# Kernel tuning notes

Hardware: AMD Instinct MI355X
Metric: run time of the kernel (lower is better)

The kernel has to match this reference:

```python
import jax, jax.numpy as jnp
import numpy as np

NUM_HEADS = 16
NUM_KV_HEADS = 4
HEAD_DIM = 128
HALF_DIM = HEAD_DIM // 2
LAMBDA_INIT = 0.8
LAMBDA_MIN = 0.0
LAMBDA_MAX = 1.0
CAUSAL = True
NORMALIZE_DIFF = True
NEG = -1.0e9


def setup_inputs() -> dict:
    key = jax.random.key(0)
    k1, k2, k3 = jax.random.split(key, 3)
    B, Sq, Sk = 1, 2048, 2048
    query = jax.random.normal(k1, (B, NUM_HEADS, Sq, HEAD_DIM), dtype=jnp.float32)
    key_t = jax.random.normal(k2, (B, NUM_KV_HEADS, Sk, HEAD_DIM), dtype=jnp.float32)
    value = jax.random.normal(k3, (B, NUM_KV_HEADS, Sk, HEAD_DIM), dtype=jnp.float32)
    return {"query": query, "key": key_t, "value": value}


def reference(query, key, value):
    scale = 1.0 / (HALF_DIM ** 0.5)
    lam = jnp.clip(jnp.float32(LAMBDA_INIT), LAMBDA_MIN, LAMBDA_MAX)
    # GQA: repeat KV heads to match query heads
    rep = NUM_HEADS // NUM_KV_HEADS
    k = jnp.repeat(key, rep, axis=1)    # [b,h,k,d]
    v = jnp.repeat(value, rep, axis=1)  # [b,h,k,d]
    q1, q2 = query[..., :HALF_DIM], query[..., HALF_DIM:]
    k1, k2 = k[..., :HALF_DIM], k[..., HALF_DIM:]
    scores1 = jnp.einsum('bhqd,bhkd->bhqk', q1, k1) * scale
    scores2 = jnp.einsum('bhqd,bhkd->bhqk', q2, k2) * scale
    if CAUSAL:
        Sq, Sk = query.shape[2], k.shape[2]
        mask = jnp.tril(jnp.ones((Sq, Sk), dtype=jnp.float32))  # lower-triangular causal
        scores1 = scores1 * mask + (1.0 - mask) * NEG
        scores2 = scores2 * mask + (1.0 - mask) * NEG
    attn1 = jax.nn.softmax(scores1, axis=-1)
    attn2 = jax.nn.softmax(scores2, axis=-1)
    diff_attn = attn1 - lam * attn2
    out = jnp.einsum('bhqk,bhkd->bhqd', diff_attn, v)
    if NORMALIZE_DIFF:
        out = out * (1.0 - LAMBDA_INIT)
    return out
```

## Files before the change

### kernel.cpp

```cpp
#include <hip/hip_runtime.h>

#define NUM_HEADS 16
#define HEAD_DIM  128
#define SEQ       2048
#define KT_STRIDE 8192

typedef __attribute__((ext_vector_type(8))) unsigned short us8;
typedef __attribute__((ext_vector_type(8))) __bf16 bf16x8;
typedef __attribute__((ext_vector_type(4))) float f32x4;
typedef __attribute__((ext_vector_type(16))) float f32x16;
typedef __attribute__((ext_vector_type(4))) unsigned u32x4;
typedef __attribute__((ext_vector_type(2))) unsigned u32x2;

static __device__ inline unsigned short f2bf(float x) {
    union { float f; unsigned u; } v; v.f = x;
    unsigned r = v.u + 0x7FFFu + ((v.u >> 16) & 1u);
    return (unsigned short)(r >> 16);
}
static __device__ inline unsigned pk2bf(float a, float b) {
    return (unsigned)f2bf(a) | ((unsigned)f2bf(b) << 16);
}
static __device__ inline float fast_exp2(float x) {
#if __has_builtin(__builtin_amdgcn_exp2f)
    return __builtin_amdgcn_exp2f(x);
#else
    return exp2f(x);
#endif
}
static __device__ inline unsigned pack_hi(unsigned clo, unsigned chi) {
#if __has_builtin(__builtin_amdgcn_perm)
    return __builtin_amdgcn_perm(chi, clo, 0x07060302u);
#else
    return (clo >> 16) | (chi & 0xffff0000u);
#endif
}
static __device__ inline f32x16 mfma32(us8 a, us8 b, f32x16 c) {
    return __builtin_amdgcn_mfma_f32_32x32x16_bf16(
        __builtin_bit_cast(bf16x8, a), __builtin_bit_cast(bf16x8, b), c, 0, 0, 0);
}

__global__ __launch_bounds__(256)
void prep_frag(const float* __restrict__ K, const float* __restrict__ V,
               unsigned short* __restrict__ KF, unsigned short* __restrict__ VF)
{
    const int bx  = (int)blockIdx.x, t = (int)threadIdx.x;
    const int which = bx & 1, khb = (bx >> 1) & 1, kt = (bx >> 2) & 31, kvh = bx >> 7;
    __shared__ __align__(16) float Ls[32][132];

    const float* src = (which ? V : K) + ((size_t)kvh * SEQ + kt * 64 + khb * 32) * HEAD_DIM;
    #pragma unroll
    for (int i = 0; i < 4; ++i) {
        const int idx = t + i * 256;
        const int r = idx >> 5, c4 = idx & 31;
        *(float4*)&Ls[r][c4 * 4] = *(const float4*)(src + (size_t)r * HEAD_DIM + c4 * 4);
    }
    __syncthreads();

    if (!which) {
        #pragma unroll
        for (int i = 0; i < 2; ++i) {
            const int c = t + i * 256;
            const int lane = c & 63, ds = (c >> 6) & 3, mat = (c >> 8) & 1;
            const int H = lane >> 5;
            const int row = lane & 31;
            const int dim = mat * 64 + ds * 16 + H * 8;
            u32x4 pk;
            #pragma unroll
            for (int jj = 0; jj < 4; ++jj)
                pk[jj] = pk2bf(Ls[row][dim + 2*jj], Ls[row][dim + 2*jj + 1]);
            *(us8*)(KF + ((size_t)(kvh * 32 + kt) * 16 + khb * 8 + mat * 4 + ds) * 512 + lane * 8)
                = __builtin_bit_cast(us8, pk);
        }
    } else {
        #pragma unroll
        for (int i = 0; i < 2; ++i) {
            const int c = t + i * 256;
            const int lane = c & 63, db = (c >> 6) & 3, ks = (c >> 8) & 1;
            const int H = lane >> 5;
            const int s0 = ks * 16 + H * 8;
            const int d  = db * 32 + (lane & 31);
            u32x4 pk;
            #pragma unroll
            for (int jj = 0; jj < 4; ++jj)
                pk[jj] = pk2bf(Ls[s0 + 2*jj][d], Ls[s0 + 2*jj + 1][d]);
            *(us8*)(VF + ((size_t)(kvh * 32 + kt) * 16 + khb * 8 + ks * 4 + db) * 512 + lane * 8)
                = __builtin_bit_cast(us8, pk);
        }
    }
}

__global__ __launch_bounds__(512, 2)
void diff_attn_mfma16(const float* __restrict__ Q,
                      const unsigned short* __restrict__ KF,
                      const unsigned short* __restrict__ VF,
                      float* __restrict__ Out)
{
    __shared__ __align__(16) unsigned short KV[3][16384];
    __shared__ float rsb[2][2][2][32];
    float* cbf = (float*)&KV[0][0];
#define CB(qs, m, qq, ii) cbf[((((qs) * 2 + (m)) * 32 + (qq)) * 136) + (ii)]

    const int t    = (int)threadIdx.x;
    const int wv   = t >> 6;
    const int ln   = t & 63;
    const int qsel = wv >> 2;
    const int mat  = (wv >> 1) & 1;
    const int kh   = wv & 1;
    const int q    = ln & 31;
    const int H    = ln >> 5;

    const int bx  = (int)blockIdx.x;
    const int xcd = bx & 7;
    const int u   = bx >> 3;
    const int kvh = xcd >> 1;
    const int h   = kvh * 4 + (u & 3);
    const int ss  = (u >> 2) | ((xcd & 1) << 3);

    const unsigned short* sgb = (wv < 4 ? KF : VF)
        + ((size_t)kvh * 32 * 16 + (wv & 3) * 4) * 512 + ln * 8;
    auto stage = [&](int jt, int b) {
        const unsigned short* tb = sgb + (size_t)jt * KT_STRIDE;
        #pragma unroll
        for (int i = 0; i < 4; ++i) {
            __builtin_amdgcn_global_load_lds(
                (const __attribute__((address_space(1))) unsigned int*)(tb + i * 512),
                (__attribute__((address_space(3))) unsigned int*)&KV[b][(wv * 4 + i) * 512],
                16, 0, 0);
        }
    };

    const int kbase = (kh * 8 + mat * 4) * 512;
    const int vbase = (16 + kh * 8) * 512;

    const float qscale = 0.125f * 1.44269504088896340736f;

    us8 qhi[4];
    auto loadQ = [&](int q0c) {
        const float* qr = Q + ((size_t)h * SEQ + q0c + q) * HEAD_DIM + mat * 64;
        #pragma unroll
        for (int ds = 0; ds < 4; ++ds) {
            const int d0 = ds * 16 + H * 8;
            float x[8];
            *(float4*)&x[0] = *(const float4*)(qr + d0);
            *(float4*)&x[4] = *(const float4*)(qr + d0 + 4);
            us8 hi8;
            #pragma unroll
            for (int j = 0; j < 8; ++j) hi8[j] = f2bf(x[j] * qscale);
            qhi[ds] = hi8;
        }
    };

    f32x16 o[4];
    f32x4  rsv;

    auto make_bp = [&](const f32x16& sv, const f32x16& sw, int rbase, int kg0, int qg,
                       bool dmask) -> us8 {
        unsigned c0[8];
        if (dmask) {
            #pragma unroll
            for (int r = 0; r < 8; ++r) {
                const int ri = rbase + r;
                const int kg = kg0 + (ri & 3) + ((ri >> 2) << 3);
                float e = (kg <= qg) ? fast_exp2(sv[ri] + sw[ri]) : 0.f;
                c0[r] = __builtin_bit_cast(unsigned, e);
            }
        } else {
            #pragma unroll
            for (int r = 0; r < 8; ++r) {
                const int ri = rbase + r;
                c0[r] = __builtin_bit_cast(unsigned, fast_exp2(sv[ri] + sw[ri]));
            }
        }
        const unsigned pA = pack_hi(c0[0], c0[1]);
        const unsigned pB = pack_hi(c0[2], c0[3]);
        const unsigned pC = pack_hi(c0[4], c0[5]);
        const unsigned pD = pack_hi(c0[6], c0[7]);
        rsv[0] += __builtin_bit_cast(float, pA << 16);
        rsv[1] += __builtin_bit_cast(float, pA & 0xffff0000u);
        rsv[2] += __builtin_bit_cast(float, pB << 16);
        rsv[3] += __builtin_bit_cast(float, pB & 0xffff0000u);
        rsv[0] += __builtin_bit_cast(float, pC << 16);
        rsv[1] += __builtin_bit_cast(float, pC & 0xffff0000u);
        rsv[2] += __builtin_bit_cast(float, pD << 16);
        rsv[3] += __builtin_bit_cast(float, pD & 0xffff0000u);
        u32x4 bw;
#if __has_builtin(__builtin_amdgcn_permlane32_swap)
        {
            u32x2 r02 = __builtin_amdgcn_permlane32_swap(pA, pC, false, false);
            u32x2 r13 = __builtin_amdgcn_permlane32_swap(pB, pD, false, false);
            bw[0] = r02[0]; bw[1] = r13[0]; bw[2] = r02[1]; bw[3] = r13[1];
        }
#else
        {
            const unsigned x1 = H ? pA : pC;
            const unsigned x2 = H ? pB : pD;
            const unsigned t1 = (unsigned)__shfl_xor((int)x1, 32, 64);
            const unsigned t2 = (unsigned)__shfl_xor((int)x2, 32, 64);
            bw[0] = H ? t1 : pA;
            bw[1] = H ? t2 : pB;
            bw[2] = H ? pC : t1;
            bw[3] = H ? pD : t2;
        }
#endif
        return __builtin_bit_cast(us8, bw);
    };

    auto epilogue = [&](int q0c) {
        __syncthreads();
        {
            float rsc = (rsv[0] + rsv[1]) + (rsv[2] + rsv[3]);
            rsc += __shfl_xor(rsc, 32, 64);
            if (ln < 32) rsb[qsel][mat][kh][ln] = rsc;
        }
        if (kh == 1) {
            #pragma unroll
            for (int db = 0; db < 4; ++db)
                #pragma unroll
                for (int i = 0; i < 4; ++i) {
                    float4 v = { o[db][i*4+0], o[db][i*4+1], o[db][i*4+2], o[db][i*4+3] };
                    *(float4*)&CB(qsel, mat, q, db * 32 + 8 * i + 4 * H) = v;
                }
        }
        __syncthreads();
        if (kh == 0) {
            const float l = rsb[qsel][mat][0][q] + rsb[qsel][mat][1][q];
            const float a = mat ? (0.16f / l) : (0.2f / l);
            #pragma unroll
            for (int db = 0; db < 4; ++db)
                #pragma unroll
                for (int i = 0; i < 4; ++i) {
                    float4 v = *(float4*)&CB(qsel, mat, q, db * 32 + 8 * i + 4 * H);
                    o[db][i*4+0] = (o[db][i*4+0] + v.x) * a;
                    o[db][i*4+1] = (o[db][i*4+1] + v.y) * a;
                    o[db][i*4+2] = (o[db][i*4+2] + v.z) * a;
                    o[db][i*4+3] = (o[db][i*4+3] + v.w) * a;
                }
            if (mat == 1) {
                #pragma unroll
                for (int db = 0; db < 4; ++db)
                    #pragma unroll
                    for (int i = 0; i < 4; ++i) {
                        float4 v = { o[db][i*4+0], o[db][i*4+1], o[db][i*4+2], o[db][i*4+3] };
                        *(float4*)&CB(qsel, 1, q, db * 32 + 8 * i + 4 * H) = v;
                    }
            }
        }
        __syncthreads();
        if (mat == 0 && kh == 0) {
            float* ob = Out + ((size_t)h * SEQ + q0c + q) * HEAD_DIM;
            #pragma unroll
            for (int db = 0; db < 4; ++db)
                #pragma unroll
                for (int i = 0; i < 4; ++i) {
                    float4 v = *(float4*)&CB(qsel, 1, q, db * 32 + 8 * i + 4 * H);
                    float4 r;
                    r.x = o[db][i*4+0] - v.x;
                    r.y = o[db][i*4+1] - v.y;
                    r.z = o[db][i*4+2] - v.z;
                    r.w = o[db][i*4+3] - v.w;
                    *(float4*)(ob + db * 32 + 8 * i + 4 * H) = r;
                }
        }
    };

    auto run_pair = [&](int p) {
        const int nseg = p + 1;
        const int q0   = p * 64 + qsel * 32;
        loadQ(q0);
        #pragma unroll
        for (int i = 0; i < 4; ++i) o[i] = (f32x16)0.f;
        rsv = (f32x4)0.f;

        __syncthreads();
        stage(0, 0);
        asm volatile("s_waitcnt vmcnt(0)" ::: "memory");
        __builtin_amdgcn_sched_barrier(0);
        __builtin_amdgcn_s_barrier();
        __builtin_amdgcn_sched_barrier(0);

        int cur = 0;
        for (int j = 0; j < nseg; ++j) {
            if (j + 1 < nseg) {
                stage(j + 1, (cur + 1) % 3);
                asm volatile("s_waitcnt vmcnt(4)" ::: "memory");
            } else {
                asm volatile("s_waitcnt vmcnt(0)" ::: "memory");
            }
            __builtin_amdgcn_sched_barrier(0);
            __builtin_amdgcn_s_barrier();
            __builtin_amdgcn_sched_barrier(0);

            const unsigned short* bufp = &KV[cur][0];
            us8 kaf[4];
            #pragma unroll
            for (int ds = 0; ds < 4; ++ds)
                kaf[ds] = *(const us8*)&bufp[kbase + ds * 512 + ln * 8];
            us8 va[8];
            #pragma unroll
            for (int c = 0; c < 8; ++c)
                va[c] = *(const us8*)&bufp[vbase + c * 512 + ln * 8];

            f32x16 s  = (f32x16)0.f;
            f32x16 s2 = (f32x16)0.f;
            s  = mfma32(kaf[0], qhi[0], s);
            s2 = mfma32(kaf[2], qhi[2], s2);
            s  = mfma32(kaf[1], qhi[1], s);
            s2 = mfma32(kaf[3], qhi[3], s2);

            const bool last = (j == nseg - 1);
            const int  kg0  = j * 64 + kh * 32 + 4 * H;
            const int  qg   = q0 + q;

            us8 bp = make_bp(s, s2, 0, kg0, qg, last);
            #pragma unroll
            for (int db = 0; db < 4; ++db) o[db] = mfma32(va[db], bp, o[db]);
            bp = make_bp(s, s2, 8, kg0, qg, last);
            #pragma unroll
            for (int db = 0; db < 4; ++db) o[db] = mfma32(va[4 + db], bp, o[db]);

            cur = (cur + 1) % 3;
        }
        epilogue(q0);
    };

    run_pair(31 - ss);
    run_pair(ss);
#undef CB
}

extern "C" void kernel_launch(void* const* d_in, const int* in_sizes, int n_in,
                              void* d_out, int out_size, void* d_ws, size_t ws_size,
                              hipStream_t stream) {
    const float* Q = (const float*)d_in[0];
    const float* K = (const float*)d_in[1];
    const float* V = (const float*)d_in[2];
    float* Out = (float*)d_out;

    unsigned short* KF = (unsigned short*)d_ws;
    unsigned short* VF = KF + (size_t)4 * SEQ * HEAD_DIM;

    prep_frag<<<512, 256, 0, stream>>>(K, V, KF, VF);
    diff_attn_mfma16<<<256, 512, 0, stream>>>(Q, KF, VF, Out);
}
```

Measured before the change: 113.8 us.

## Process two KV tiles per barrier with double-buffered pairs and MFMA priority

```diff
diff --git a/kernel.cpp b/kernel.cpp
--- a/kernel.cpp
+++ b/kernel.cpp
@@ -90,14 +90,14 @@
 }
 
 __global__ __launch_bounds__(512, 2)
-void diff_attn_mfma16(const float* __restrict__ Q,
+void diff_attn_mfma18(const float* __restrict__ Q,
                       const unsigned short* __restrict__ KF,
                       const unsigned short* __restrict__ VF,
                       float* __restrict__ Out)
 {
-    __shared__ __align__(16) unsigned short KV[3][16384];
+    __shared__ __align__(16) unsigned short KV[2][2][16384];
     __shared__ float rsb[2][2][2][32];
-    float* cbf = (float*)&KV[0][0];
+    float* cbf = (float*)&KV[0][0][0];
 #define CB(qs, m, qq, ii) cbf[((((qs) * 2 + (m)) * 32 + (qq)) * 136) + (ii)]
 
     const int t    = (int)threadIdx.x;
@@ -118,13 +118,13 @@
 
     const unsigned short* sgb = (wv < 4 ? KF : VF)
         + ((size_t)kvh * 32 * 16 + (wv & 3) * 4) * 512 + ln * 8;
-    auto stage = [&](int jt, int b) {
+    auto stage = [&](int jt, int b, int hf) {
         const unsigned short* tb = sgb + (size_t)jt * KT_STRIDE;
         #pragma unroll
         for (int i = 0; i < 4; ++i) {
             __builtin_amdgcn_global_load_lds(
                 (const __attribute__((address_space(1))) unsigned int*)(tb + i * 512),
-                (__attribute__((address_space(3))) unsigned int*)&KV[b][(wv * 4 + i) * 512],
+                (__attribute__((address_space(3))) unsigned int*)&KV[b][hf][(wv * 4 + i) * 512],
                 16, 0, 0);
         }
     };
@@ -264,61 +264,97 @@
     };
 
     auto run_pair = [&](int p) {
-        const int nseg = p + 1;
-        const int q0   = p * 64 + qsel * 32;
+        const int nseg  = p + 1;
+        const int nbody = (nseg + 1) >> 1;
+        const int q0    = p * 64 + qsel * 32;
         loadQ(q0);
         #pragma unroll
         for (int i = 0; i < 4; ++i) o[i] = (f32x16)0.f;
         rsv = (f32x4)0.f;
 
         __syncthreads();
-        stage(0, 0);
-        asm volatile("s_waitcnt vmcnt(0)" ::: "memory");
-        __builtin_amdgcn_sched_barrier(0);
-        __builtin_amdgcn_s_barrier();
-        __builtin_amdgcn_sched_barrier(0);
-
-        int cur = 0;
-        for (int j = 0; j < nseg; ++j) {
-            if (j + 1 < nseg) {
-                stage(j + 1, (cur + 1) % 3);
-                asm volatile("s_waitcnt vmcnt(4)" ::: "memory");
-            } else {
-                asm volatile("s_waitcnt vmcnt(0)" ::: "memory");
-            }
+        stage(0, 0, 0);
+        if (nseg > 1) stage(1, 0, 1);
+
+        int bc = 0;
+        const int qg = q0 + q;
+        for (int jb = 0; jb < nbody; ++jb) {
+            const int t0 = 2 * jb, t1 = t0 + 1;
+            const bool has1 = (t1 < nseg);
+
+            asm volatile("s_waitcnt vmcnt(0)" ::: "memory");
             __builtin_amdgcn_sched_barrier(0);
             __builtin_amdgcn_s_barrier();
             __builtin_amdgcn_sched_barrier(0);
 
-            const unsigned short* bufp = &KV[cur][0];
-            us8 kaf[4];
+            if (t0 + 2 < nseg) stage(t0 + 2, bc ^ 1, 0);
+            if (t1 + 2 < nseg) stage(t1 + 2, bc ^ 1, 1);
+
+            const unsigned short* b0 = &KV[bc][0][0];
+            const unsigned short* b1 = &KV[bc][1][0];
+
+            us8 kaf0[4], va0[8];
             #pragma unroll
             for (int ds = 0; ds < 4; ++ds)
-                kaf[ds] = *(const us8*)&bufp[kbase + ds * 512 + ln * 8];
-            us8 va[8];
+                kaf0[ds] = *(const us8*)&b0[kbase + ds * 512 + ln * 8];
             #pragma unroll
             for (int c = 0; c < 8; ++c)
-                va[c] = *(const us8*)&bufp[vbase + c * 512 + ln * 8];
-
-            f32x16 s  = (f32x16)0.f;
-            f32x16 s2 = (f32x16)0.f;
-            s  = mfma32(kaf[0], qhi[0], s);
-            s2 = mfma32(kaf[2], qhi[2], s2);
-            s  = mfma32(kaf[1], qhi[1], s);
-            s2 = mfma32(kaf[3], qhi[3], s2);
-
-            const bool last = (j == nseg - 1);
-            const int  kg0  = j * 64 + kh * 32 + 4 * H;
-            const int  qg   = q0 + q;
-
-            us8 bp = make_bp(s, s2, 0, kg0, qg, last);
-            #pragma unroll
-            for (int db = 0; db < 4; ++db) o[db] = mfma32(va[db], bp, o[db]);
-            bp = make_bp(s, s2, 8, kg0, qg, last);
-            #pragma unroll
-            for (int db = 0; db < 4; ++db) o[db] = mfma32(va[4 + db], bp, o[db]);
-
-            cur = (cur + 1) % 3;
+                va0[c] = *(const us8*)&b0[vbase + c * 512 + ln * 8];
+            us8 kaf1[4], va1[8];
+            if (has1) {
+                #pragma unroll
+                for (int ds = 0; ds < 4; ++ds)
+                    kaf1[ds] = *(const us8*)&b1[kbase + ds * 512 + ln * 8];
+                #pragma unroll
+                for (int c = 0; c < 8; ++c)
+                    va1[c] = *(const us8*)&b1[vbase + c * 512 + ln * 8];
+            }
+
+            f32x16 sA = (f32x16)0.f, sB = (f32x16)0.f;
+            f32x16 sC = (f32x16)0.f, sD = (f32x16)0.f;
+            __builtin_amdgcn_s_setprio(1);
+            sA = mfma32(kaf0[0], qhi[0], sA);
+            sB = mfma32(kaf0[2], qhi[2], sB);
+            sA = mfma32(kaf0[1], qhi[1], sA);
+            sB = mfma32(kaf0[3], qhi[3], sB);
+            if (has1) {
+                sC = mfma32(kaf1[0], qhi[0], sC);
+                sD = mfma32(kaf1[2], qhi[2], sD);
+                sC = mfma32(kaf1[1], qhi[1], sC);
+                sD = mfma32(kaf1[3], qhi[3], sD);
+            }
+            __builtin_amdgcn_s_setprio(0);
+
+            {
+                const bool l0  = (t0 == nseg - 1);
+                const int  kg0 = t0 * 64 + kh * 32 + 4 * H;
+                us8 bp = make_bp(sA, sB, 0, kg0, qg, l0);
+                __builtin_amdgcn_s_setprio(1);
+                #pragma unroll
+                for (int db = 0; db < 4; ++db) o[db] = mfma32(va0[db], bp, o[db]);
+                __builtin_amdgcn_s_setprio(0);
+                bp = make_bp(sA, sB, 8, kg0, qg, l0);
+                __builtin_amdgcn_s_setprio(1);
+                #pragma unroll
+                for (int db = 0; db < 4; ++db) o[db] = mfma32(va0[4 + db], bp, o[db]);
+                __builtin_amdgcn_s_setprio(0);
+            }
+            if (has1) {
+                const bool l1  = (t1 == nseg - 1);
+                const int  kg1 = t1 * 64 + kh * 32 + 4 * H;
+                us8 bp = make_bp(sC, sD, 0, kg1, qg, l1);
+                __builtin_amdgcn_s_setprio(1);
+                #pragma unroll
+                for (int db = 0; db < 4; ++db) o[db] = mfma32(va1[db], bp, o[db]);
+                __builtin_amdgcn_s_setprio(0);
+                bp = make_bp(sC, sD, 8, kg1, qg, l1);
+                __builtin_amdgcn_s_setprio(1);
+                #pragma unroll
+                for (int db = 0; db < 4; ++db) o[db] = mfma32(va1[4 + db], bp, o[db]);
+                __builtin_amdgcn_s_setprio(0);
+            }
+
+            bc ^= 1;
         }
         epilogue(q0);
     };
@@ -340,5 +376,5 @@
     unsigned short* VF = KF + (size_t)4 * SEQ * HEAD_DIM;
 
     prep_frag<<<512, 256, 0, stream>>>(K, V, KF, VF);
-    diff_attn_mfma16<<<256, 512, 0, stream>>>(Q, KF, VF, Out);
-}
+    diff_attn_mfma18<<<256, 512, 0, stream>>>(Q, KF, VF, Out);
+}
```

Result: slower. 124.6 us (+9.5%).
